# Optimization experiments

Hardware: AMD Instinct MI355X
Metric: run time of the kernel (lower is better)

## Reference

```python
import jax, jax.numpy as jnp
import numpy as np

H_RES, W_RES = 32, 32
DIM = 512
NUM_HEADS = 16
HEAD_DIM = DIM // NUM_HEADS
SCALE = HEAD_DIM ** -0.5
B = 16
N = H_RES * W_RES
TABLE_SIZE = (2 * H_RES - 1) * (2 * W_RES - 1)


def _relative_position_index():
    coords_h = np.arange(H_RES)
    coords_w = np.arange(W_RES)
    coords = np.stack(np.meshgrid(coords_h, coords_w, indexing='ij'))  # [2, H, W]
    coords_flat = coords.reshape(2, -1)  # [2, N]
    rel = coords_flat[:, :, None] - coords_flat[:, None, :]  # [2, N, N]
    rel = rel.transpose(1, 2, 0).astype(np.int64)  # [N, N, 2]
    rel[:, :, 0] += H_RES - 1
    rel[:, :, 1] += W_RES - 1
    rel[:, :, 0] *= 2 * W_RES - 1
    return rel.sum(-1)  # [N, N]


def setup_inputs() -> dict:
    key = jax.random.key(0)
    ks = jax.random.split(key, 6)
    x = jax.random.normal(ks[0], (B, N, DIM), dtype=jnp.float32)
    w_qkv = jax.random.normal(ks[1], (DIM, 3 * DIM), dtype=jnp.float32) * (DIM ** -0.5)
    b_qkv = jnp.zeros((3 * DIM,), dtype=jnp.float32)
    w_proj = jax.random.normal(ks[2], (DIM, DIM), dtype=jnp.float32) * (DIM ** -0.5)
    b_proj = jnp.zeros((DIM,), dtype=jnp.float32)
    bias_table = jax.random.normal(ks[3], (TABLE_SIZE, NUM_HEADS), dtype=jnp.float32) * 0.02
    rel_index = jnp.asarray(_relative_position_index(), dtype=jnp.int32)
    return {"x": x, "w_qkv": w_qkv, "b_qkv": b_qkv, "w_proj": w_proj,
            "b_proj": b_proj, "bias_table": bias_table, "rel_index": rel_index}


def reference(x, w_qkv, b_qkv, w_proj, b_proj, bias_table, rel_index):
    Bq, Nq, C = x.shape
    qkv = x @ w_qkv + b_qkv  # [B, N, 3C]
    qkv = qkv.reshape(Bq, Nq, 3, NUM_HEADS, HEAD_DIM)
    q = qkv[:, :, 0].transpose(0, 2, 1, 3) * SCALE  # [B, nH, N, d]
    k = qkv[:, :, 1].transpose(0, 2, 1, 3)
    v = qkv[:, :, 2].transpose(0, 2, 1, 3)
    attn = jnp.einsum('bhnd,bhmd->bhnm', q, k)  # [B, nH, N, N]
    bias = bias_table[rel_index]  # [N, N, nH]
    attn = attn + bias.transpose(2, 0, 1)[None]  # broadcast over batch
    attn = jax.nn.softmax(attn, axis=-1)
    out = jnp.einsum('bhnm,bhmd->bhnd', attn, v)  # [B, nH, N, d]
    out = out.transpose(0, 2, 1, 3).reshape(Bq, Nq, C)
    return out @ w_proj + b_proj
```

## Files before the change

kernel.cpp:

```cpp
#include <hip/hip_runtime.h>
#include <hip/hip_bf16.h>
#include <cstdint>
#include <cstddef>

typedef _Float16 f16;
typedef __attribute__((ext_vector_type(8))) _Float16 f16x8;
typedef __attribute__((ext_vector_type(2))) _Float16 f16x2;
typedef __bf16 bf16;
typedef __attribute__((ext_vector_type(4))) float f32x4;
typedef __attribute__((ext_vector_type(16))) float f32x16;

#define LOG2E 1.4426950408889634f
#define QK_SCALE 0.17677669529663687f

__device__ __forceinline__ f32x4 mfma16f(f16x8 a, f16x8 b, f32x4 c) {
  return __builtin_amdgcn_mfma_f32_16x16x32_f16(a, b, c, 0, 0, 0);
}
__device__ __forceinline__ f32x16 mfma32f(f16x8 a, f16x8 b, f32x16 c) {
  return __builtin_amdgcn_mfma_f32_32x32x16_f16(a, b, c, 0, 0, 0);
}
__device__ __forceinline__ float exp2_hw(float x) {
  float r; asm("v_exp_f32 %0, %1" : "=v"(r) : "v"(x)); return r;
}
__device__ __forceinline__ uint32_t cvtpk_f16(float a, float b) {
  uint32_t r; asm("v_cvt_pkrtz_f16_f32 %0, %1, %2" : "=v"(r) : "v"(a), "v"(b)); return r;
}
__device__ __forceinline__ float lo16f(uint32_t u) { return __uint_as_float(u << 16); }
__device__ __forceinline__ float hi16raw(uint32_t u) { return __uint_as_float(u); }

__device__ __forceinline__ float dot2acc(uint32_t u, float acc) {
  union { uint32_t x; f16x2 h; } c; c.x = u;
  f16x2 one2 = {(_Float16)1.0f, (_Float16)1.0f};
  return __builtin_amdgcn_fdot2(c.h, one2, acc, false);
}

__device__ __forceinline__ void gl16(const f16* g, f16* l) {
  __builtin_amdgcn_global_load_lds(
      (const __attribute__((address_space(1))) void*)g,
      (__attribute__((address_space(3))) void*)l, 16, 0, 0);
}

__device__ __forceinline__ uint32_t packoff(int m, int k) {
  return (((uint32_t)(m >> 7) * 16u + (uint32_t)(k >> 5)) * 8u + (uint32_t)((m >> 4) & 7)) * 512u
       + (uint32_t)((k >> 3) & 3) * 128u + (uint32_t)(m & 15) * 8u + (uint32_t)(k & 7);
}

__global__ __launch_bounds__(256) void prep_kernel(
    const float* __restrict__ x, const float* __restrict__ wqkv, const float* __restrict__ wproj,
    const float* __restrict__ btab,
    f16* __restrict__ Xp, f16* __restrict__ Wq, f16* __restrict__ Wp,
    bf16* __restrict__ biasC)
{
  const int XT  = 16384 * 512 / 16;
  const int WQT = 1536 * 512 / 16;
  const int WPT = 512 * 512 / 16;
  int t = blockIdx.x * 256 + threadIdx.x;
  if (t < XT) {
    uint32_t o = (uint32_t)t * 16u;
    uint32_t blk = o >> 9, rem = o & 511u;
    uint32_t k23 = rem >> 7, r16 = (rem >> 3) & 15u;
    uint32_t i7 = blk & 7u, k5 = (blk >> 3) & 15u, m7 = blk >> 7;
    uint32_t m = m7 * 128u + i7 * 16u + r16;
    uint32_t k = k5 * 32u + k23 * 8u;
    const float* s0 = x + (size_t)m * 512 + k;
    f32x4 a0 = *(const f32x4*)s0;
    f32x4 a1 = *(const f32x4*)(s0 + 4);
    f32x4 b0 = *(const f32x4*)(s0 + 512);
    f32x4 b1 = *(const f32x4*)(s0 + 516);
    f16 ov[16];
    #pragma unroll
    for (int j = 0; j < 4; ++j) {
      ov[j] = (f16)a0[j]; ov[4 + j] = (f16)a1[j];
      ov[8 + j] = (f16)b0[j]; ov[12 + j] = (f16)b1[j];
    }
    *(uint4*)(Xp + o) = *(uint4*)&ov[0];
    *(uint4*)(Xp + o + 8) = *(uint4*)&ov[8];
  } else if (t < XT + WQT) {
    uint32_t o = (uint32_t)(t - XT) * 16u;
    uint32_t blk = o >> 9, rem = o & 511u;
    uint32_t k23 = rem >> 7, r16 = (rem >> 3) & 15u;
    uint32_t i7 = blk & 7u, k5 = (blk >> 3) & 15u, m7 = blk >> 7;
    uint32_t n = m7 * 128u + i7 * 16u + r16;
    uint32_t k = k5 * 32u + k23 * 8u;
    f16 ov[16];
    #pragma unroll
    for (int j = 0; j < 8; ++j) {
      ov[j] = (f16)wqkv[(size_t)(k + j) * 1536 + n];
      ov[8 + j] = (f16)wqkv[(size_t)(k + j) * 1536 + n + 1];
    }
    *(uint4*)(Wq + o) = *(uint4*)&ov[0];
    *(uint4*)(Wq + o + 8) = *(uint4*)&ov[8];
  } else if (t < XT + WQT + WPT) {
    uint32_t o = (uint32_t)(t - XT - WQT) * 16u;
    uint32_t blk = o >> 9, rem = o & 511u;
    uint32_t k23 = rem >> 7, r16 = (rem >> 3) & 15u;
    uint32_t i7 = blk & 7u, k5 = (blk >> 3) & 15u, m7 = blk >> 7;
    uint32_t n = m7 * 128u + i7 * 16u + r16;
    uint32_t k = k5 * 32u + k23 * 8u;
    f16 ov[16];
    #pragma unroll
    for (int j = 0; j < 8; ++j) {
      ov[j] = (f16)wproj[(size_t)(k + j) * 512 + n];
      ov[8 + j] = (f16)wproj[(size_t)(k + j) * 512 + n + 1];
    }
    *(uint4*)(Wp + o) = *(uint4*)&ov[0];
    *(uint4*)(Wp + o + 8) = *(uint4*)&ov[8];
  } else {
    int t2 = t - (XT + WQT + WPT);
    if (t2 < 16 * 63 * 64) {
      int lane = t2 & 63;
      int sh = t2 >> 6;
      int s = sh % 63, h = sh / 63;
      int lq = lane & 31, hi5 = lane >> 5;
      int base = s * 63 + 31 + lq;
      bf16 o[16];
      #pragma unroll
      for (int r = 0; r < 16; ++r) {
        int kx = (r & 3) + 8 * (r >> 2) + 4 * hi5;
        o[r] = (bf16)(btab[(base - kx) * 16 + h] * LOG2E);
      }
      *(uint4*)(biasC + (size_t)t2 * 16) = *(uint4*)&o[0];
      *(uint4*)(biasC + (size_t)t2 * 16 + 8) = *(uint4*)&o[8];
    }
  }
}

template<int NB>
__global__ __launch_bounds__(256) void gemm_frag(
    const f16* __restrict__ Ap, const f16* __restrict__ Bp,
    const float* __restrict__ bvec,
    f16* __restrict__ Qp, f16* __restrict__ Kp, f16* __restrict__ Vt,
    float* __restrict__ out)
{
  __shared__ f16 sA[3][4096];
  __shared__ f16 sB[3][4096];
  const int bid = blockIdx.x;
  const int xcd = bid & 7, idx = bid >> 3;
  int mb, nb;
  if (NB == 12) { int q = idx / 12; mb = xcd * 16 + q; nb = idx - q * 12; }
  else          { mb = xcd * 16 + (idx >> 2); nb = idx & 3; }
  const int tid = threadIdx.x, lane = tid & 63, wave = tid >> 6;
  const int l15 = lane & 15, l4 = lane >> 4;
  const int wr = wave >> 1, wc = wave & 1;

  const f16* gA = Ap + (uint32_t)mb * 65536u + (uint32_t)wave * 1024u + (uint32_t)lane * 8u;
  const f16* gB = Bp + (uint32_t)nb * 65536u + (uint32_t)wave * 1024u + (uint32_t)lane * 8u;
  const int wl = wave * 1024;

  gl16(gA,        &sA[0][wl]);
  gl16(gA + 512,  &sA[0][wl + 512]);
  gl16(gB,        &sB[0][wl]);
  gl16(gB + 512,  &sB[0][wl + 512]);
  gl16(gA + 4096, &sA[1][wl]);
  gl16(gA + 4608, &sA[1][wl + 512]);
  gl16(gB + 4096, &sB[1][wl]);
  gl16(gB + 4608, &sB[1][wl + 512]);

  f32x4 acc[4][4];
  #pragma unroll
  for (int i = 0; i < 4; ++i)
    #pragma unroll
    for (int j = 0; j < 4; ++j) acc[i][j] = (f32x4){0.f, 0.f, 0.f, 0.f};

  const uint32_t aoff = (uint32_t)(wr * 4) * 512u + (uint32_t)lane * 8u;
  const uint32_t boff = (uint32_t)(wc * 4) * 512u + (uint32_t)lane * 8u;

  #pragma unroll
  for (int kt = 0; kt < 16; ++kt) {
    asm volatile("s_waitcnt vmcnt(4)" ::: "memory");
    asm volatile("s_barrier" ::: "memory");
    const int s2 = (kt + 2) % 3;
    gl16(gA + (kt + 2) * 4096,       &sA[s2][wl]);
    gl16(gA + (kt + 2) * 4096 + 512, &sA[s2][wl + 512]);
    gl16(gB + (kt + 2) * 4096,       &sB[s2][wl]);
    gl16(gB + (kt + 2) * 4096 + 512, &sB[s2][wl + 512]);
    __builtin_amdgcn_sched_barrier(0);
    const int s0 = kt % 3;
    f16x8 af[4], bfr[4];
    #pragma unroll
    for (int f = 0; f < 4; ++f) {
      af[f]  = *(const f16x8*)&sA[s0][aoff + f * 512];
      bfr[f] = *(const f16x8*)&sB[s0][boff + f * 512];
    }
    #pragma unroll
    for (int mf = 0; mf < 4; ++mf)
      #pragma unroll
      for (int nf = 0; nf < 4; ++nf)
        acc[mf][nf] = mfma16f(af[mf], bfr[nf], acc[mf][nf]);
  }
  asm volatile("s_waitcnt vmcnt(0)" ::: "memory");

  #pragma unroll
  for (int mf = 0; mf < 4; ++mf) {
    #pragma unroll
    for (int nf = 0; nf < 4; ++nf) {
      int colb = nb * 128 + wc * 64 + nf * 16 + l15;
      float bb = bvec[colb];
      #pragma unroll
      for (int i = 0; i < 4; ++i) {
        int m = mb * 128 + wr * 64 + mf * 16 + l4 * 4 + i;
        float v = acc[mf][nf][i] + bb;
        if (NB == 4) {
          out[(size_t)m * 512 + colb] = v;
        } else {
          int t = colb >> 9, cc = colb & 511;
          int b = m >> 10, n = m & 1023;
          int hh = cc >> 5, d = cc & 31;
          int bh2 = b * 16 + hh;
          if (t == 0) {
            v *= (QK_SCALE * LOG2E);
            uint32_t off = (((uint32_t)bh2 * 32u + (uint32_t)(n >> 5)) * 2u + (uint32_t)(d >> 4)) * 512u
                         + ((uint32_t)((d >> 3) & 1) * 32u + (uint32_t)(n & 31)) * 8u + (uint32_t)(d & 7);
            Qp[off] = (f16)v;
          } else if (t == 1) {
            Kp[((size_t)(bh2 * 2 + (d >> 4)) * 1024 + n) * 16 + (d & 15)] = (f16)v;
          } else {
            int nl = n & 15;
            int npl = (nl >= 4 && nl < 12) ? (nl ^ 12) : nl;
            int np = (n & ~15) | npl;
            Vt[((size_t)(bh2 * 128 + (np >> 3)) * 32 + d) * 8 + (np & 7)] = (f16)v;
          }
        }
      }
    }
  }
}

__global__ __launch_bounds__(256) void attn_kernel(
    const f16* __restrict__ Qp, const f16* __restrict__ Kp, const f16* __restrict__ Vt,
    const bf16* __restrict__ biasC, f16* __restrict__ Op)
{
  const int bid = blockIdx.x;
  const int xcd = bid & 7, slot = bid >> 3;
  const int h = xcd * 2 + (slot >> 6);
  const int rest = slot & 63;
  const int qg = rest >> 4, b = rest & 15;
  const int bh = b * 16 + h;
  const int tid = threadIdx.x, lane = tid & 63, wave = tid >> 6;
  const int lq = lane & 31, hi5 = lane >> 5;

  const int qb0 = qg * 8 + wave * 2;
  const int m0 = b * 1024 + qb0 * 32;

  const uint32_t qbase = ((uint32_t)bh * 32u + (uint32_t)qb0) * 1024u + (uint32_t)lane * 8u;
  const f16x8 q00 = *(const f16x8*)(Qp + qbase);
  const f16x8 q01 = *(const f16x8*)(Qp + qbase + 512);
  const f16x8 q10 = *(const f16x8*)(Qp + qbase + 1024);
  const f16x8 q11 = *(const f16x8*)(Qp + qbase + 1536);

  uint32_t koff = (uint32_t)bh * 32768u + (uint32_t)lq * 16u + (uint32_t)hi5 * 8u;
  uint32_t voff = (uint32_t)bh * 32768u + (uint32_t)hi5 * 256u + (uint32_t)lq * 8u;
  const bf16* bp = biasC + ((uint32_t)(h * 63 + qb0 + 31) * 64u + (uint32_t)lane) * 16u;

  f16x8 kA0 = *(const f16x8*)(Kp + koff);
  f16x8 kA1 = *(const f16x8*)(Kp + koff + 16384);
  uint4 p0A = *(const uint4*)(bp);
  uint4 p1A = *(const uint4*)(bp + 8);
  uint4 p2A = *(const uint4*)(bp + 1024);
  uint4 p3A = *(const uint4*)(bp + 1032);
  f16x8 vA0 = *(const f16x8*)(Vt + voff);
  f16x8 vA1 = *(const f16x8*)(Vt + voff + 512);
  f16x8 kB0 = *(const f16x8*)(Kp + koff + 512);
  f16x8 kB1 = *(const f16x8*)(Kp + koff + 16384 + 512);
  uint4 p0B = *(const uint4*)(bp - 1024);
  uint4 p1B = *(const uint4*)(bp - 1016);
  uint4 p2B = *(const uint4*)(bp);
  uint4 p3B = *(const uint4*)(bp + 8);
  f16x8 vB0 = *(const f16x8*)(Vt + voff + 1024);
  f16x8 vB1 = *(const f16x8*)(Vt + voff + 1536);

  f32x16 O0, O1;
  #pragma unroll
  for (int i = 0; i < 16; ++i) { O0[i] = 0.f; O1[i] = 0.f; }
  f32x4 racc0 = {0.f, 0.f, 0.f, 0.f}, racc1 = {0.f, 0.f, 0.f, 0.f};

  union Uf { uint32_t u[4]; f16x8 v; };

#define UNPACK16(S, Pa, Pb)                               \
  S[0]  = lo16f(Pa.x); S[1]  = hi16raw(Pa.x);             \
  S[2]  = lo16f(Pa.y); S[3]  = hi16raw(Pa.y);             \
  S[4]  = lo16f(Pa.z); S[5]  = hi16raw(Pa.z);             \
  S[6]  = lo16f(Pa.w); S[7]  = hi16raw(Pa.w);             \
  S[8]  = lo16f(Pb.x); S[9]  = hi16raw(Pb.x);             \
  S[10] = lo16f(Pb.y); S[11] = hi16raw(Pb.y);             \
  S[12] = lo16f(Pb.z); S[13] = hi16raw(Pb.z);             \
  S[14] = lo16f(Pb.w); S[15] = hi16raw(Pb.w);

  auto tile = [&](f16x8& K0, f16x8& K1, f16x8& V0, f16x8& V1,
                  uint4& P0, uint4& P1, uint4& P2, uint4& P3,
                  uint32_t kpre, uint32_t vpre, int bpre) {
    asm volatile("s_waitcnt vmcnt(8)" ::: "memory");
    f32x16 S0, S1;
    UNPACK16(S0, P0, P1)
    UNPACK16(S1, P2, P3)
    S0 = mfma32f(K0, q00, S0);
    S0 = mfma32f(K1, q01, S0);
    S1 = mfma32f(K0, q10, S1);
    S1 = mfma32f(K1, q11, S1);
    K0 = *(const f16x8*)(Kp + koff + kpre);
    K1 = *(const f16x8*)(Kp + koff + 16384 + kpre);
    P0 = *(const uint4*)(bp + bpre);
    P1 = *(const uint4*)(bp + bpre + 8);
    P2 = *(const uint4*)(bp + bpre + 1024);
    P3 = *(const uint4*)(bp + bpre + 1032);
    __builtin_amdgcn_sched_barrier(0);
    {
      float e0  = exp2_hw(S0[0]),  e1  = exp2_hw(S0[1]),  e2  = exp2_hw(S0[2]),  e3  = exp2_hw(S0[3]);
      float e4  = exp2_hw(S0[4]),  e5  = exp2_hw(S0[5]),  e6  = exp2_hw(S0[6]),  e7  = exp2_hw(S0[7]);
      float e8  = exp2_hw(S0[8]),  e9  = exp2_hw(S0[9]),  e10 = exp2_hw(S0[10]), e11 = exp2_hw(S0[11]);
      float e12 = exp2_hw(S0[12]), e13 = exp2_hw(S0[13]), e14 = exp2_hw(S0[14]), e15 = exp2_hw(S0[15]);
      Uf a1, a2;
      a1.u[0] = cvtpk_f16(e0,  e1);  a1.u[1] = cvtpk_f16(e2,  e3);
      a1.u[2] = cvtpk_f16(e4,  e5);  a1.u[3] = cvtpk_f16(e6,  e7);
      a2.u[0] = cvtpk_f16(e8,  e9);  a2.u[1] = cvtpk_f16(e10, e11);
      a2.u[2] = cvtpk_f16(e12, e13); a2.u[3] = cvtpk_f16(e14, e15);
      racc0[0] = dot2acc(a1.u[0], racc0[0]); racc0[1] = dot2acc(a1.u[1], racc0[1]);
      racc0[2] = dot2acc(a1.u[2], racc0[2]); racc0[3] = dot2acc(a1.u[3], racc0[3]);
      racc0[0] = dot2acc(a2.u[0], racc0[0]); racc0[1] = dot2acc(a2.u[1], racc0[1]);
      racc0[2] = dot2acc(a2.u[2], racc0[2]); racc0[3] = dot2acc(a2.u[3], racc0[3]);
      O0 = mfma32f(a1.v, V0, O0);
      O0 = mfma32f(a2.v, V1, O0);
    }
    {
      float e0  = exp2_hw(S1[0]),  e1  = exp2_hw(S1[1]),  e2  = exp2_hw(S1[2]),  e3  = exp2_hw(S1[3]);
      float e4  = exp2_hw(S1[4]),  e5  = exp2_hw(S1[5]),  e6  = exp2_hw(S1[6]),  e7  = exp2_hw(S1[7]);
      float e8  = exp2_hw(S1[8]),  e9  = exp2_hw(S1[9]),  e10 = exp2_hw(S1[10]), e11 = exp2_hw(S1[11]);
      float e12 = exp2_hw(S1[12]), e13 = exp2_hw(S1[13]), e14 = exp2_hw(S1[14]), e15 = exp2_hw(S1[15]);
      Uf a1, a2;
      a1.u[0] = cvtpk_f16(e0,  e1);  a1.u[1] = cvtpk_f16(e2,  e3);
      a1.u[2] = cvtpk_f16(e4,  e5);  a1.u[3] = cvtpk_f16(e6,  e7);
      a2.u[0] = cvtpk_f16(e8,  e9);  a2.u[1] = cvtpk_f16(e10, e11);
      a2.u[2] = cvtpk_f16(e12, e13); a2.u[3] = cvtpk_f16(e14, e15);
      racc1[0] = dot2acc(a1.u[0], racc1[0]); racc1[1] = dot2acc(a1.u[1], racc1[1]);
      racc1[2] = dot2acc(a1.u[2], racc1[2]); racc1[3] = dot2acc(a1.u[3], racc1[3]);
      racc1[0] = dot2acc(a2.u[0], racc1[0]); racc1[1] = dot2acc(a2.u[1], racc1[1]);
      racc1[2] = dot2acc(a2.u[2], racc1[2]); racc1[3] = dot2acc(a2.u[3], racc1[3]);
      O1 = mfma32f(a1.v, V0, O1);
      O1 = mfma32f(a2.v, V1, O1);
    }
    V0 = *(const f16x8*)(Vt + voff + vpre);
    V1 = *(const f16x8*)(Vt + voff + vpre + 512);
    __builtin_amdgcn_sched_barrier(0);
  };

  #pragma unroll 1
  for (int it = 0; it < 16; ++it) {
    tile(kA0, kA1, vA0, vA1, p0A, p1A, p2A, p3A, 1024u, 2048u, -2048);
    tile(kB0, kB1, vB0, vB1, p0B, p1B, p2B, p3B, 1536u, 3072u, -3072);
    koff += 1024u; voff += 2048u; bp -= 2048;
  }

  float rs0 = (racc0[0] + racc0[1]) + (racc0[2] + racc0[3]);
  rs0 += __shfl_xor(rs0, 32);
  float inv0 = 1.0f / rs0;
  float rs1 = (racc1[0] + racc1[1]) + (racc1[2] + racc1[3]);
  rs1 += __shfl_xor(rs1, 32);
  float inv1 = 1.0f / rs1;

  const int kcol = h * 32 + lq;
  #pragma unroll
  for (int r = 0; r < 16; ++r) {
    int qrow = (r & 3) + 8 * (r >> 2) + 4 * hi5;
    float t0 = __shfl(inv0, qrow);
    float t1 = __shfl(inv1, qrow);
    Op[packoff(m0 + qrow, kcol)] = (f16)(O0[r] * t0);
    Op[packoff(m0 + 32 + qrow, kcol)] = (f16)(O1[r] * t1);
  }
}

extern "C" void kernel_launch(void* const* d_in, const int* in_sizes, int n_in,
                              void* d_out, int out_size, void* d_ws, size_t ws_size,
                              hipStream_t stream) {
  const float* x     = (const float*)d_in[0];
  const float* wqkv  = (const float*)d_in[1];
  const float* bqkv  = (const float*)d_in[2];
  const float* wproj = (const float*)d_in[3];
  const float* bproj = (const float*)d_in[4];
  const float* btab  = (const float*)d_in[5];
  float* out = (float*)d_out;

  char* ws = (char*)d_ws;
  size_t off = 0;
  auto walloc = [&](size_t bytes) {
    void* p = ws + off;
    off += (bytes + 255) & ~(size_t)255;
    return p;
  };
  const size_t PAD = 262144;
  f16* Xp   = (f16*)walloc((size_t)16384 * 512 * 2 + PAD);
  f16* Wq   = (f16*)walloc((size_t)1536 * 512 * 2 + PAD);
  f16* Wp   = (f16*)walloc((size_t)512 * 512 * 2 + PAD);
  f16* Qp   = (f16*)walloc((size_t)16384 * 512 * 2 + PAD);
  f16* Kp   = (f16*)walloc((size_t)16384 * 512 * 2 + PAD);
  f16* Vt   = (f16*)walloc((size_t)16384 * 512 * 2 + PAD);
  bf16* biasC = (bf16*)walloc((size_t)16 * 63 * 64 * 16 * 2 + PAD);
  f16* Op   = (f16*)walloc((size_t)16384 * 512 * 2 + PAD);

  const int prep_total = 16384 * 512 / 16 + 1536 * 512 / 16 + 512 * 512 / 16 + 16 * 63 * 64;
  prep_kernel<<<(prep_total + 255) / 256, 256, 0, stream>>>(
      x, wqkv, wproj, btab, Xp, Wq, Wp, biasC);

  gemm_frag<12><<<1536, 256, 0, stream>>>(
      Xp, Wq, bqkv, Qp, Kp, Vt, nullptr);

  attn_kernel<<<1024, 256, 0, stream>>>(Qp, Kp, Vt, biasC, Op);

  gemm_frag<4><<<512, 256, 0, stream>>>(
      Op, Wp, bproj, nullptr, nullptr, nullptr, out);
}
```

Before: 150.3 us.

## Store attention bias as fp32 and feed it directly as MFMA accumulator

The relative-position bias is now precomputed in fp32 rather than bf16, so the attention kernel loads it straight into the MFMA accumulator registers and skips the per-element unpack. The bias prefetch is reorganised into even/odd register sets with a changed vmcnt wait, and the kernel gets a waves-per-EU launch-bounds hint. The x conversion in the prep kernel now handles 32 elements per thread with coalesced row reads. In exchange the bias traffic doubles and more bias registers are live per tile, which adds register pressure.

```diff
diff --git a/kernel.cpp b/kernel.cpp
--- a/kernel.cpp
+++ b/kernel.cpp
@@ -6,7 +6,6 @@
 typedef _Float16 f16;
 typedef __attribute__((ext_vector_type(8))) _Float16 f16x8;
 typedef __attribute__((ext_vector_type(2))) _Float16 f16x2;
-typedef __bf16 bf16;
 typedef __attribute__((ext_vector_type(4))) float f32x4;
 typedef __attribute__((ext_vector_type(16))) float f32x16;
 
@@ -25,8 +24,6 @@
 __device__ __forceinline__ uint32_t cvtpk_f16(float a, float b) {
   uint32_t r; asm("v_cvt_pkrtz_f16_f32 %0, %1, %2" : "=v"(r) : "v"(a), "v"(b)); return r;
 }
-__device__ __forceinline__ float lo16f(uint32_t u) { return __uint_as_float(u << 16); }
-__device__ __forceinline__ float hi16raw(uint32_t u) { return __uint_as_float(u); }
 
 __device__ __forceinline__ float dot2acc(uint32_t u, float acc) {
   union { uint32_t x; f16x2 h; } c; c.x = u;
@@ -49,34 +46,41 @@
     const float* __restrict__ x, const float* __restrict__ wqkv, const float* __restrict__ wproj,
     const float* __restrict__ btab,
     f16* __restrict__ Xp, f16* __restrict__ Wq, f16* __restrict__ Wp,
-    bf16* __restrict__ biasC)
+    float* __restrict__ biasF)
 {
-  const int XT  = 16384 * 512 / 16;
+  const int XT2 = 16384 * 512 / 32;
   const int WQT = 1536 * 512 / 16;
   const int WPT = 512 * 512 / 16;
   int t = blockIdx.x * 256 + threadIdx.x;
-  if (t < XT) {
-    uint32_t o = (uint32_t)t * 16u;
-    uint32_t blk = o >> 9, rem = o & 511u;
-    uint32_t k23 = rem >> 7, r16 = (rem >> 3) & 15u;
-    uint32_t i7 = blk & 7u, k5 = (blk >> 3) & 15u, m7 = blk >> 7;
-    uint32_t m = m7 * 128u + i7 * 16u + r16;
-    uint32_t k = k5 * 32u + k23 * 8u;
-    const float* s0 = x + (size_t)m * 512 + k;
+  if (t < XT2) {
+    uint32_t rp = (uint32_t)t >> 5;
+    uint32_t kk = ((uint32_t)t & 31u) << 4;
+    uint32_t me = rp << 1;
+    const float* s0 = x + (size_t)me * 512 + kk;
+    const float* s1 = s0 + 512;
     f32x4 a0 = *(const f32x4*)s0;
     f32x4 a1 = *(const f32x4*)(s0 + 4);
-    f32x4 b0 = *(const f32x4*)(s0 + 512);
-    f32x4 b1 = *(const f32x4*)(s0 + 516);
-    f16 ov[16];
+    f32x4 a2 = *(const f32x4*)(s0 + 8);
+    f32x4 a3 = *(const f32x4*)(s0 + 12);
+    f32x4 b0 = *(const f32x4*)s1;
+    f32x4 b1 = *(const f32x4*)(s1 + 4);
+    f32x4 b2 = *(const f32x4*)(s1 + 8);
+    f32x4 b3 = *(const f32x4*)(s1 + 12);
+    uint32_t o = packoff(me, kk);
+    f16 r0[8], r1[8], r2[8], r3[8];
     #pragma unroll
     for (int j = 0; j < 4; ++j) {
-      ov[j] = (f16)a0[j]; ov[4 + j] = (f16)a1[j];
-      ov[8 + j] = (f16)b0[j]; ov[12 + j] = (f16)b1[j];
-    }
-    *(uint4*)(Xp + o) = *(uint4*)&ov[0];
-    *(uint4*)(Xp + o + 8) = *(uint4*)&ov[8];
-  } else if (t < XT + WQT) {
-    uint32_t o = (uint32_t)(t - XT) * 16u;
+      r0[j] = (f16)a0[j]; r0[4 + j] = (f16)a1[j];
+      r1[j] = (f16)b0[j]; r1[4 + j] = (f16)b1[j];
+      r2[j] = (f16)a2[j]; r2[4 + j] = (f16)a3[j];
+      r3[j] = (f16)b2[j]; r3[4 + j] = (f16)b3[j];
+    }
+    *(uint4*)(Xp + o)       = *(uint4*)&r0[0];
+    *(uint4*)(Xp + o + 8)   = *(uint4*)&r1[0];
+    *(uint4*)(Xp + o + 128) = *(uint4*)&r2[0];
+    *(uint4*)(Xp + o + 136) = *(uint4*)&r3[0];
+  } else if (t < XT2 + WQT) {
+    uint32_t o = (uint32_t)(t - XT2) * 16u;
     uint32_t blk = o >> 9, rem = o & 511u;
     uint32_t k23 = rem >> 7, r16 = (rem >> 3) & 15u;
     uint32_t i7 = blk & 7u, k5 = (blk >> 3) & 15u, m7 = blk >> 7;
@@ -90,8 +94,8 @@
     }
     *(uint4*)(Wq + o) = *(uint4*)&ov[0];
     *(uint4*)(Wq + o + 8) = *(uint4*)&ov[8];
-  } else if (t < XT + WQT + WPT) {
-    uint32_t o = (uint32_t)(t - XT - WQT) * 16u;
+  } else if (t < XT2 + WQT + WPT) {
+    uint32_t o = (uint32_t)(t - XT2 - WQT) * 16u;
     uint32_t blk = o >> 9, rem = o & 511u;
     uint32_t k23 = rem >> 7, r16 = (rem >> 3) & 15u;
     uint32_t i7 = blk & 7u, k5 = (blk >> 3) & 15u, m7 = blk >> 7;
@@ -106,21 +110,24 @@
     *(uint4*)(Wp + o) = *(uint4*)&ov[0];
     *(uint4*)(Wp + o + 8) = *(uint4*)&ov[8];
   } else {
-    int t2 = t - (XT + WQT + WPT);
+    int t2 = t - (XT2 + WQT + WPT);
     if (t2 < 16 * 63 * 64) {
       int lane = t2 & 63;
       int sh = t2 >> 6;
       int s = sh % 63, h = sh / 63;
       int lq = lane & 31, hi5 = lane >> 5;
       int base = s * 63 + 31 + lq;
-      bf16 o[16];
+      float o[16];
       #pragma unroll
       for (int r = 0; r < 16; ++r) {
         int kx = (r & 3) + 8 * (r >> 2) + 4 * hi5;
-        o[r] = (bf16)(btab[(base - kx) * 16 + h] * LOG2E);
+        o[r] = btab[(base - kx) * 16 + h] * LOG2E;
       }
-      *(uint4*)(biasC + (size_t)t2 * 16) = *(uint4*)&o[0];
-      *(uint4*)(biasC + (size_t)t2 * 16 + 8) = *(uint4*)&o[8];
+      float* dst = biasF + (size_t)t2 * 16;
+      *(uint4*)(dst)      = *(uint4*)&o[0];
+      *(uint4*)(dst + 4)  = *(uint4*)&o[4];
+      *(uint4*)(dst + 8)  = *(uint4*)&o[8];
+      *(uint4*)(dst + 12) = *(uint4*)&o[12];
     }
   }
 }
@@ -226,9 +233,9 @@
   }
 }
 
-__global__ __launch_bounds__(256) void attn_kernel(
+__global__ __launch_bounds__(256, 4) void attn_kernel(
     const f16* __restrict__ Qp, const f16* __restrict__ Kp, const f16* __restrict__ Vt,
-    const bf16* __restrict__ biasC, f16* __restrict__ Op)
+    const float* __restrict__ biasF, f16* __restrict__ Op)
 {
   const int bid = blockIdx.x;
   const int xcd = bid & 7, slot = bid >> 3;
@@ -250,22 +257,25 @@
 
   uint32_t koff = (uint32_t)bh * 32768u + (uint32_t)lq * 16u + (uint32_t)hi5 * 8u;
   uint32_t voff = (uint32_t)bh * 32768u + (uint32_t)hi5 * 256u + (uint32_t)lq * 8u;
-  const bf16* bp = biasC + ((uint32_t)(h * 63 + qb0 + 31) * 64u + (uint32_t)lane) * 16u;
-
+  const float* bpf = biasF + (uint32_t)(h * 63 + qb0 + 31) * 1024u + (uint32_t)lane * 16u;
+
+  union Ub { f32x16 v; f32x4 q[4]; };
+  Ub Ue0, Ue1, Uo0, Uo1;
+
+  Ue0.q[0] = *(const f32x4*)(bpf);
+  Ue0.q[1] = *(const f32x4*)(bpf + 4);
+  Ue0.q[2] = *(const f32x4*)(bpf + 8);
+  Ue0.q[3] = *(const f32x4*)(bpf + 12);
+  Ue1.q[0] = *(const f32x4*)(bpf + 1024);
+  Ue1.q[1] = *(const f32x4*)(bpf + 1028);
+  Ue1.q[2] = *(const f32x4*)(bpf + 1032);
+  Ue1.q[3] = *(const f32x4*)(bpf + 1036);
   f16x8 kA0 = *(const f16x8*)(Kp + koff);
   f16x8 kA1 = *(const f16x8*)(Kp + koff + 16384);
-  uint4 p0A = *(const uint4*)(bp);
-  uint4 p1A = *(const uint4*)(bp + 8);
-  uint4 p2A = *(const uint4*)(bp + 1024);
-  uint4 p3A = *(const uint4*)(bp + 1032);
   f16x8 vA0 = *(const f16x8*)(Vt + voff);
   f16x8 vA1 = *(const f16x8*)(Vt + voff + 512);
   f16x8 kB0 = *(const f16x8*)(Kp + koff + 512);
   f16x8 kB1 = *(const f16x8*)(Kp + koff + 16384 + 512);
-  uint4 p0B = *(const uint4*)(bp - 1024);
-  uint4 p1B = *(const uint4*)(bp - 1016);
-  uint4 p2B = *(const uint4*)(bp);
-  uint4 p3B = *(const uint4*)(bp + 8);
   f16x8 vB0 = *(const f16x8*)(Vt + voff + 1024);
   f16x8 vB1 = *(const f16x8*)(Vt + voff + 1536);
 
@@ -276,33 +286,24 @@
 
   union Uf { uint32_t u[4]; f16x8 v; };
 
-#define UNPACK16(S, Pa, Pb)                               \
-  S[0]  = lo16f(Pa.x); S[1]  = hi16raw(Pa.x);             \
-  S[2]  = lo16f(Pa.y); S[3]  = hi16raw(Pa.y);             \
-  S[4]  = lo16f(Pa.z); S[5]  = hi16raw(Pa.z);             \
-  S[6]  = lo16f(Pa.w); S[7]  = hi16raw(Pa.w);             \
-  S[8]  = lo16f(Pb.x); S[9]  = hi16raw(Pb.x);             \
-  S[10] = lo16f(Pb.y); S[11] = hi16raw(Pb.y);             \
-  S[12] = lo16f(Pb.z); S[13] = hi16raw(Pb.z);             \
-  S[14] = lo16f(Pb.w); S[15] = hi16raw(Pb.w);
-
   auto tile = [&](f16x8& K0, f16x8& K1, f16x8& V0, f16x8& V1,
-                  uint4& P0, uint4& P1, uint4& P2, uint4& P3,
-                  uint32_t kpre, uint32_t vpre, int bpre) {
-    asm volatile("s_waitcnt vmcnt(8)" ::: "memory");
-    f32x16 S0, S1;
-    UNPACK16(S0, P0, P1)
-    UNPACK16(S1, P2, P3)
-    S0 = mfma32f(K0, q00, S0);
+                  Ub& Uc0, Ub& Uc1, Ub& Un0, Ub& Un1,
+                  uint32_t kpre, uint32_t vpre, int bn0, int bn1) {
+    asm volatile("s_waitcnt vmcnt(4)" ::: "memory");
+    f32x16 S0 = mfma32f(K0, q00, Uc0.v);
     S0 = mfma32f(K1, q01, S0);
-    S1 = mfma32f(K0, q10, S1);
+    f32x16 S1 = mfma32f(K0, q10, Uc1.v);
     S1 = mfma32f(K1, q11, S1);
+    Un0.q[0] = *(const f32x4*)(bpf + bn0);
+    Un0.q[1] = *(const f32x4*)(bpf + bn0 + 4);
+    Un0.q[2] = *(const f32x4*)(bpf + bn0 + 8);
+    Un0.q[3] = *(const f32x4*)(bpf + bn0 + 12);
+    Un1.q[0] = *(const f32x4*)(bpf + bn1);
+    Un1.q[1] = *(const f32x4*)(bpf + bn1 + 4);
+    Un1.q[2] = *(const f32x4*)(bpf + bn1 + 8);
+    Un1.q[3] = *(const f32x4*)(bpf + bn1 + 12);
     K0 = *(const f16x8*)(Kp + koff + kpre);
     K1 = *(const f16x8*)(Kp + koff + 16384 + kpre);
-    P0 = *(const uint4*)(bp + bpre);
-    P1 = *(const uint4*)(bp + bpre + 8);
-    P2 = *(const uint4*)(bp + bpre + 1024);
-    P3 = *(const uint4*)(bp + bpre + 1032);
     __builtin_amdgcn_sched_barrier(0);
     {
       float e0  = exp2_hw(S0[0]),  e1  = exp2_hw(S0[1]),  e2  = exp2_hw(S0[2]),  e3  = exp2_hw(S0[3]);
@@ -345,9 +346,9 @@
 
   #pragma unroll 1
   for (int it = 0; it < 16; ++it) {
-    tile(kA0, kA1, vA0, vA1, p0A, p1A, p2A, p3A, 1024u, 2048u, -2048);
-    tile(kB0, kB1, vB0, vB1, p0B, p1B, p2B, p3B, 1536u, 3072u, -3072);
-    koff += 1024u; voff += 2048u; bp -= 2048;
+    tile(kA0, kA1, vA0, vA1, Ue0, Ue1, Uo0, Uo1, 1024u, 2048u, -1024, 0);
+    tile(kB0, kB1, vB0, vB1, Uo0, Uo1, Ue0, Ue1, 1536u, 3072u, -2048, -1024);
+    koff += 1024u; voff += 2048u; bpf -= 2048;
   }
 
   float rs0 = (racc0[0] + racc0[1]) + (racc0[2] + racc0[3]);
@@ -393,17 +394,17 @@
   f16* Qp   = (f16*)walloc((size_t)16384 * 512 * 2 + PAD);
   f16* Kp   = (f16*)walloc((size_t)16384 * 512 * 2 + PAD);
   f16* Vt   = (f16*)walloc((size_t)16384 * 512 * 2 + PAD);
-  bf16* biasC = (bf16*)walloc((size_t)16 * 63 * 64 * 16 * 2 + PAD);
+  float* biasF = (float*)walloc((size_t)16 * 63 * 64 * 16 * 4 + PAD);
   f16* Op   = (f16*)walloc((size_t)16384 * 512 * 2 + PAD);
 
-  const int prep_total = 16384 * 512 / 16 + 1536 * 512 / 16 + 512 * 512 / 16 + 16 * 63 * 64;
+  const int prep_total = 16384 * 512 / 32 + 1536 * 512 / 16 + 512 * 512 / 16 + 16 * 63 * 64;
   prep_kernel<<<(prep_total + 255) / 256, 256, 0, stream>>>(
-      x, wqkv, wproj, btab, Xp, Wq, Wp, biasC);
+      x, wqkv, wproj, btab, Xp, Wq, Wp, biasF);
 
   gemm_frag<12><<<1536, 256, 0, stream>>>(
       Xp, Wq, bqkv, Qp, Kp, Vt, nullptr);
 
-  attn_kernel<<<1024, 256, 0, stream>>>(Qp, Kp, Vt, biasC, Op);
+  attn_kernel<<<1024, 256, 0, stream>>>(Qp, Kp, Vt, biasF, Op);
 
   gemm_frag<4><<<512, 256, 0, stream>>>(
       Op, Wp, bproj, nullptr, nullptr, nullptr, out);
```

New measurement: 339.6 us. 2.26x slower.
